# Optimization experiments

Hardware: AMD Instinct MI355X
Metric: run time of the kernel (lower is better)

The kernel has to match this reference:

```python
import jax, jax.numpy as jnp
import numpy as np

V = 50001   # vocab_size = len(word2id)+1
E = 256     # embedding_dim
H = 512     # hidden_dim (bi-LSTM output)
HD = 256    # hidden per direction = hidden_dim // 2
K = 9       # tagset_size
B = 64
T = 256


def setup_inputs() -> dict:
    key = jax.random.key(0)
    ks = jax.random.split(key, 16)
    n = lambda k, shape, s: (jax.random.normal(k, shape, jnp.float32) * s)
    inp = {
        "x": jax.random.randint(ks[0], (B, T), 0, V - 1),
        "embed": n(ks[1], (V, E), 0.1),
        # torch LSTM weights: gate order [i, f, g, o], each [4*HD, in]
        "w_ih_f": n(ks[2], (4 * HD, E), 0.05),
        "w_hh_f": n(ks[3], (4 * HD, HD), 0.05),
        "b_ih_f": n(ks[4], (4 * HD,), 0.05),
        "b_hh_f": n(ks[5], (4 * HD,), 0.05),
        "w_ih_b": n(ks[6], (4 * HD, E), 0.05),
        "w_hh_b": n(ks[7], (4 * HD, HD), 0.05),
        "b_ih_b": n(ks[8], (4 * HD,), 0.05),
        "b_hh_b": n(ks[9], (4 * HD,), 0.05),
        "w_out": n(ks[10], (K, H), 0.05),
        "b_out": n(ks[11], (K,), 0.05),
        "crf_start": n(ks[12], (K,), 0.1),
        "crf_end": n(ks[13], (K,), 0.1),
        "crf_trans": n(ks[14], (K, K), 0.1),
    }
    return inp


def _lstm_dir(xs, w_ih, w_hh, b_ih, b_hh, reverse):
    # xs: [T, B, E] -> hs: [T, B, HD]
    bsz = xs.shape[1]
    hd = w_hh.shape[1]
    b = b_ih + b_hh

    def step(carry, xt):
        h, c = carry
        g = xt @ w_ih.T + h @ w_hh.T + b
        i, f, gg, o = jnp.split(g, 4, axis=-1)
        c = jax.nn.sigmoid(f) * c + jax.nn.sigmoid(i) * jnp.tanh(gg)
        h = jax.nn.sigmoid(o) * jnp.tanh(c)
        return (h, c), h

    init = (jnp.zeros((bsz, hd), xs.dtype), jnp.zeros((bsz, hd), xs.dtype))
    _, hs = jax.lax.scan(step, init, xs, reverse=reverse)
    return hs


def _viterbi(emissions, start, trans, end):
    # emissions: [T, B, K] -> (best_score [B], path [B, T])
    score0 = start[None, :] + emissions[0]  # [B, K]

    def fwd(score, em_t):
        # score[b, i] + trans[i, j] + em_t[b, j]
        cand = score[:, :, None] + trans[None, :, :] + em_t[:, None, :]
        return jnp.max(cand, axis=1), jnp.argmax(cand, axis=1)  # [B,K], [B,K]

    final, history = jax.lax.scan(fwd, score0, emissions[1:])
    final = final + end[None, :]
    best_score = jnp.max(final, axis=-1)        # [B]
    last_tag = jnp.argmax(final, axis=-1)       # [B]

    def back(tag, hist_t):
        prev = jnp.take_along_axis(hist_t, tag[:, None], axis=1)[:, 0]
        return prev, prev

    _, tags_rev = jax.lax.scan(back, last_tag, history, reverse=True)
    path = jnp.concatenate([tags_rev, last_tag[None, :]], axis=0)  # [T, B]
    return best_score, path.T.astype(jnp.int32)


def reference(x, embed, w_ih_f, w_hh_f, b_ih_f, b_hh_f,
              w_ih_b, w_hh_b, b_ih_b, b_hh_b,
              w_out, b_out, crf_start, crf_end, crf_trans):
    xt = x.T                           # [T, B] time-major
    emb = embed[xt]                    # [T, B, E]
    h_f = _lstm_dir(emb, w_ih_f, w_hh_f, b_ih_f, b_hh_f, reverse=False)
    h_b = _lstm_dir(emb, w_ih_b, w_hh_b, b_ih_b, b_hh_b, reverse=True)
    h = jnp.concatenate([h_f, h_b], axis=-1)          # [T, B, H]
    # dropout is identity at inference (decode)
    emissions = jnp.einsum("tbh,kh->tbk", h, w_out) + b_out  # [T, B, K]
    best_score, path = _viterbi(emissions, crf_start, crf_trans, crf_end)
    return path, best_score
```

## Files before the change

kernel.cpp:

```cpp
#include <hip/hip_runtime.h>
#include <hip/hip_bf16.h>
#include <math.h>

#define VOCAB 50001
#define EDIM 256
#define HDIM 256
#define GDIM 1024
#define KTAG 9
#define NB 64
#define NT 256

static constexpr size_t XP_OFF   = 0;
static constexpr size_t HX_OFF   = XP_OFF + (size_t)16384*2048;
static constexpr size_t BIAS_OFF = HX_OFF + 131072;
static constexpr size_t HS_OFF   = BIAS_OFF + 2048;
static constexpr size_t EM_OFF   = HS_OFF + (size_t)16384*512;

#define FMA4(acc, W, H) acc += (W).x*(H).x + (W).y*(H).y + (W).z*(H).z + (W).w*(H).w

__global__ __launch_bounds__(256) void k_prep(const float* __restrict__ bif,
                                              const float* __restrict__ bhf,
                                              const float* __restrict__ bib,
                                              const float* __restrict__ bhb,
                                              float* __restrict__ ws) {
    int t = blockIdx.x * 256 + threadIdx.x;
    float* bias = ws + BIAS_OFF;
    if (t < 2048) {
        int d = t >> 10, g = t & 1023;
        bias[t] = d ? (bib[g] + bhb[g]) : (bif[g] + bhf[g]);
    }
    unsigned long long* hx = (unsigned long long*)(ws + HX_OFF);
    for (int i = t; i < 65536; i += 4096) hx[i] = 0ull;
}

#define BKC 32
__global__ __launch_bounds__(256) void k_xproj(const int* __restrict__ x,
                                               const float* __restrict__ embed,
                                               const float* __restrict__ wih_f,
                                               const float* __restrict__ wih_b,
                                               float* __restrict__ ws) {
    float* xp = ws + XP_OFF;
    const float* bias = ws + BIAS_OFF;
    __shared__ float As[BKC][68];
    __shared__ float Bs[BKC][68];
    __shared__ int ids[64];
    const int bm = blockIdx.x;
    const int bn = blockIdx.y;
    const int tid = threadIdx.x;
    const int tx = tid & 15, ty = tid >> 4;

    if (tid < 64) {
        int r = bm * 64 + tid;
        int t = r >> 6, b = r & 63;
        ids[tid] = x[b * 256 + t];
    }
    __syncthreads();

    float acc[4][4];
#pragma unroll
    for (int i = 0; i < 4; ++i)
#pragma unroll
        for (int j = 0; j < 4; ++j) acc[i][j] = 0.f;

    const int lm = tid >> 2;
    const int lks = (tid & 3) * 8;

    for (int k0 = 0; k0 < 256; k0 += BKC) {
        {
            const float* src = embed + (size_t)ids[lm] * 256 + k0 + lks;
            float4 a0 = *reinterpret_cast<const float4*>(src);
            float4 a1 = *reinterpret_cast<const float4*>(src + 4);
            As[lks + 0][lm] = a0.x; As[lks + 1][lm] = a0.y;
            As[lks + 2][lm] = a0.z; As[lks + 3][lm] = a0.w;
            As[lks + 4][lm] = a1.x; As[lks + 5][lm] = a1.y;
            As[lks + 6][lm] = a1.z; As[lks + 7][lm] = a1.w;
        }
        {
            int gn = bn * 64 + lm;
            const float* wsrc = (gn < 1024) ? (wih_f + (size_t)gn * 256)
                                            : (wih_b + (size_t)(gn - 1024) * 256);
            const float* src = wsrc + k0 + lks;
            float4 b0 = *reinterpret_cast<const float4*>(src);
            float4 b1 = *reinterpret_cast<const float4*>(src + 4);
            Bs[lks + 0][lm] = b0.x; Bs[lks + 1][lm] = b0.y;
            Bs[lks + 2][lm] = b0.z; Bs[lks + 3][lm] = b0.w;
            Bs[lks + 4][lm] = b1.x; Bs[lks + 5][lm] = b1.y;
            Bs[lks + 6][lm] = b1.z; Bs[lks + 7][lm] = b1.w;
        }
        __syncthreads();
#pragma unroll
        for (int k = 0; k < BKC; ++k) {
            float4 a = *reinterpret_cast<const float4*>(&As[k][ty * 4]);
            float4 bq = *reinterpret_cast<const float4*>(&Bs[k][tx * 4]);
            acc[0][0] += a.x * bq.x; acc[0][1] += a.x * bq.y; acc[0][2] += a.x * bq.z; acc[0][3] += a.x * bq.w;
            acc[1][0] += a.y * bq.x; acc[1][1] += a.y * bq.y; acc[1][2] += a.y * bq.z; acc[1][3] += a.y * bq.w;
            acc[2][0] += a.z * bq.x; acc[2][1] += a.z * bq.y; acc[2][2] += a.z * bq.z; acc[2][3] += a.z * bq.w;
            acc[3][0] += a.w * bq.x; acc[3][1] += a.w * bq.y; acc[3][2] += a.w * bq.z; acc[3][3] += a.w * bq.w;
        }
        __syncthreads();
    }

    const int gm = bm * 64 + ty * 4;
    const int gn = bn * 64 + tx * 4;
#pragma unroll
    for (int i = 0; i < 4; ++i) {
        float4 o;
        o.x = acc[i][0] + bias[gn + 0];
        o.y = acc[i][1] + bias[gn + 1];
        o.z = acc[i][2] + bias[gn + 2];
        o.w = acc[i][3] + bias[gn + 3];
        *reinterpret_cast<float4*>(xp + (size_t)(gm + i) * 2048 + gn) = o;
    }
}

#define WV 23
#define WL 9
#define REC_LDS_FLOATS (WL * 1024 * 4 + 256 + 512 + 512)

__global__ __launch_bounds__(1024)
__attribute__((amdgpu_waves_per_eu(4, 4)))
void k_rec3(const float* __restrict__ whh_f,
            const float* __restrict__ whh_b,
            float* __restrict__ ws) {
    extern __shared__ float sm[];
    float4* wlds4 = reinterpret_cast<float4*>(sm);
    float* hbuf = sm + WL * 1024 * 4;
    float* gact = hbuf + 256;
    float* psum = gact + 512;

    const float* xp = ws + XP_OFF;
    unsigned long long* hx = (unsigned long long*)(ws + HX_OFF);
    float* hs = ws + HS_OFF;

    const int blk = blockIdx.x;
    const int jhalf = blk >> 7;
    const int dir = (blk >> 6) & 1;
    const int batch = blk & 63;
    const int partner = blk ^ 128;
    const int t = threadIdx.x;
    const int kh = t >> 9;
    const int rr = t & 511;
    const int gt = rr >> 7;
    const int jj = rr & 127;
    const int row_global = gt * 256 + jhalf * 128 + jj;
    const int col = dir * 1024 + row_global;
    const float* wrow = (dir ? whh_b : whh_f) + (size_t)row_global * 256 + kh * 128;

    float4 w4[WV];
#pragma unroll
    for (int i = 0; i < WV; ++i) w4[i] = reinterpret_cast<const float4*>(wrow)[i];
#pragma unroll
    for (int c = 0; c < WL; ++c)
        wlds4[c * 1024 + t] = reinterpret_cast<const float4*>(wrow)[WV + c];

    if (t < 256) hbuf[t] = 0.f;
    float creg = 0.f;
    __syncthreads();

    const long xstep = dir ? -131072 : 131072;
    const long hstep = dir ? -32768 : 32768;
    const float* xptr = xp + (size_t)(dir ? 255 : 0) * 131072 + (size_t)batch * 2048 + col;
    float* hsptr = hs + (size_t)(dir ? 255 : 0) * 32768 + (size_t)batch * 512
                   + dir * 256 + jhalf * 128 + t;
    float xpv = (t < 512) ? *xptr : 0.f;

    for (int s = 0; s < 256; ++s) {
        const float* hk = hbuf + kh * 128;

        float a0 = 0.f, a1 = 0.f, a2 = 0.f, a3 = 0.f;
#pragma unroll
        for (int q = 0; q < WV; q += 4) {
            float4 h4;
            h4 = *reinterpret_cast<const float4*>(hk + (q + 0) * 4);
            FMA4(a0, w4[q + 0], h4);
            if (q + 1 < WV) { h4 = *reinterpret_cast<const float4*>(hk + (q + 1) * 4); FMA4(a1, w4[q + 1], h4); }
            if (q + 2 < WV) { h4 = *reinterpret_cast<const float4*>(hk + (q + 2) * 4); FMA4(a2, w4[q + 2], h4); }
            if (q + 3 < WV) { h4 = *reinterpret_cast<const float4*>(hk + (q + 3) * 4); FMA4(a3, w4[q + 3], h4); }
        }
#pragma unroll
        for (int c = 0; c < WL; ++c) {
            float4 h4 = *reinterpret_cast<const float4*>(hk + (WV + c) * 4);
            float4 wl = wlds4[c * 1024 + t];
            if ((c & 3) == 0) FMA4(a0, wl, h4);
            else if ((c & 3) == 1) FMA4(a1, wl, h4);
            else if ((c & 3) == 2) FMA4(a2, wl, h4);
            else FMA4(a3, wl, h4);
        }
        const float a = (a0 + a1) + (a2 + a3);

        if (kh) psum[rr] = a;
        __syncthreads();

        if (t < 512) {
            const float acc = xpv + a + psum[t];
            const float act = (gt == 2) ? tanhf(acc) : 1.f / (1.f + expf(-acc));
            gact[t] = act;
        }
        __syncthreads();

        if (t < 128) {
            const float si = gact[t], sf = gact[128 + t], tg = gact[256 + t], so = gact[384 + t];
            creg = sf * creg + si * tg;
            const float hval = so * tanhf(creg);
            const unsigned long long pk =
                ((unsigned long long)(unsigned)(s + 1) << 32) | (unsigned)__float_as_uint(hval);
            __hip_atomic_store(&hx[((size_t)(s & 1) * 256 + blk) * 128 + t], pk,
                               __ATOMIC_RELAXED, __HIP_MEMORY_SCOPE_AGENT);
            hbuf[jhalf * 128 + t] = hval;
            *hsptr = hval;
            hsptr += hstep;
        }

        if (t < 512 && s < 255) { xptr += xstep; xpv = *xptr; }

        if (t < 128) {
            unsigned long long u;
            do {
                u = __hip_atomic_load(&hx[((size_t)(s & 1) * 256 + partner) * 128 + t],
                                      __ATOMIC_RELAXED, __HIP_MEMORY_SCOPE_AGENT);
            } while ((unsigned)(u >> 32) != (unsigned)(s + 1));
            hbuf[(1 - jhalf) * 128 + t] = __uint_as_float((unsigned)u);
        }
        __syncthreads();
    }
}

__global__ __launch_bounds__(256) void k_emis(const float* __restrict__ wout,
                                              const float* __restrict__ bout,
                                              float* __restrict__ ws) {
    const float* hs = ws + HS_OFF;
    float* em = ws + EM_OFF;
    __shared__ float wl[9][512];
    __shared__ float bl[9];
    const int tid = threadIdx.x;
    for (int i = tid; i < 9 * 512; i += 256) wl[i / 512][i % 512] = wout[i];
    if (tid < 9) bl[tid] = bout[tid];
    __syncthreads();

    const int r = blockIdx.x * 256 + tid;
    const float4* hrow = reinterpret_cast<const float4*>(hs + (size_t)r * 512);
    float acc[9];
#pragma unroll
    for (int j = 0; j < 9; ++j) acc[j] = bl[j];
    for (int k4 = 0; k4 < 128; ++k4) {
        float4 h = hrow[k4];
#pragma unroll
        for (int j = 0; j < 9; ++j) {
            float4 w = *reinterpret_cast<const float4*>(&wl[j][k4 * 4]);
            acc[j] += h.x * w.x + h.y * w.y + h.z * w.z + h.w * w.w;
        }
    }
#pragma unroll
    for (int j = 0; j < 9; ++j) em[(size_t)r * 9 + j] = acc[j];
}

__global__ __launch_bounds__(64) void k_vit(const float* __restrict__ start,
                                            const float* __restrict__ endv,
                                            const float* __restrict__ trans,
                                            const float* __restrict__ ws_c,
                                            float* __restrict__ out) {
    const float* em = ws_c + EM_OFF;
    const int b = blockIdx.x;
    const int lane = threadIdx.x;
    __shared__ float tr[81];
    __shared__ float sc[9];
    __shared__ float ns[9];
    __shared__ int hist[256][9];

    for (int i = lane; i < 81; i += 64) tr[i] = trans[i];
    if (lane < 9) sc[lane] = start[lane] + em[(size_t)b * 9 + lane];
    __syncthreads();

    for (int t = 1; t < 256; ++t) {
        if (lane < 9) {
            float e = em[((size_t)t * 64 + b) * 9 + lane];
            float best = -1e30f; int bi = 0;
#pragma unroll
            for (int i = 0; i < 9; ++i) {
                float v = sc[i] + tr[i * 9 + lane];
                if (v > best) { best = v; bi = i; }
            }
            ns[lane] = best + e;
            hist[t][lane] = bi;
        }
        __syncthreads();
        if (lane < 9) sc[lane] = ns[lane];
        __syncthreads();
    }

    if (lane == 0) {
        float best = -1e30f; int bi = 0;
        for (int j = 0; j < 9; ++j) {
            float v = sc[j] + endv[j];
            if (v > best) { best = v; bi = j; }
        }
        out[16384 + b] = best;
        int cur = bi;
        out[(size_t)b * 256 + 255] = (float)cur;
        for (int t = 255; t >= 1; --t) {
            cur = hist[t][cur];
            out[(size_t)b * 256 + t - 1] = (float)cur;
        }
    }
}

extern "C" void kernel_launch(void* const* d_in, const int* in_sizes, int n_in,
                              void* d_out, int out_size, void* d_ws, size_t ws_size,
                              hipStream_t stream) {
    (void)in_sizes; (void)n_in; (void)out_size; (void)ws_size;
    const int*   x       = (const int*)d_in[0];
    const float* embed   = (const float*)d_in[1];
    const float* w_ih_f  = (const float*)d_in[2];
    const float* w_hh_f  = (const float*)d_in[3];
    const float* b_ih_f  = (const float*)d_in[4];
    const float* b_hh_f  = (const float*)d_in[5];
    const float* w_ih_b  = (const float*)d_in[6];
    const float* w_hh_b  = (const float*)d_in[7];
    const float* b_ih_b  = (const float*)d_in[8];
    const float* b_hh_b  = (const float*)d_in[9];
    const float* w_out   = (const float*)d_in[10];
    const float* b_out   = (const float*)d_in[11];
    const float* crf_start = (const float*)d_in[12];
    const float* crf_end   = (const float*)d_in[13];
    const float* crf_trans = (const float*)d_in[14];
    float* ws  = (float*)d_ws;
    float* out = (float*)d_out;

    const size_t rec_lds_bytes = (size_t)REC_LDS_FLOATS * 4;
    hipFuncSetAttribute(reinterpret_cast<const void*>(k_rec3),
                        hipFuncAttributeMaxDynamicSharedMemorySize,
                        (int)rec_lds_bytes);

    hipLaunchKernelGGL(k_prep, dim3(16), dim3(256), 0, stream,
                       b_ih_f, b_hh_f, b_ih_b, b_hh_b, ws);
    hipLaunchKernelGGL(k_xproj, dim3(256, 32), dim3(256), 0, stream,
                       x, embed, w_ih_f, w_ih_b, ws);
    hipLaunchKernelGGL(k_rec3, dim3(256), dim3(1024), rec_lds_bytes, stream,
                       w_hh_f, w_hh_b, ws);
    hipLaunchKernelGGL(k_emis, dim3(64), dim3(256), 0, stream, w_out, b_out, ws);
    hipLaunchKernelGGL(k_vit, dim3(64), dim3(64), 0, stream,
                       crf_start, crf_end, crf_trans, ws, out);
}
```

Before: 998.2 us.

## Process two batch elements per recurrent block to reuse register-held weights

The recurrent LSTM kernel now handles two batch rows per block, so each weight fragment held in registers and LDS serves two matvecs per timestep. The grid drops from 256 to 128 blocks, and the h-exchange buffers, gate buffers and cell states are duplicated. This amortises weight reads and the per-step barrier and partner-exchange cost over more work. In exchange each step has roughly twice the FMA and LDS-read work per block, and more register pressure at a fixed 4 waves/EU.

```diff
diff --git a/kernel.cpp b/kernel.cpp
--- a/kernel.cpp
+++ b/kernel.cpp
@@ -115,7 +115,7 @@
 
 #define WV 23
 #define WL 9
-#define REC_LDS_FLOATS (WL * 1024 * 4 + 256 + 512 + 512)
+#define REC_LDS_FLOATS (WL * 1024 * 4 + 2 * (256 + 512 + 512))
 
 __global__ __launch_bounds__(1024)
 __attribute__((amdgpu_waves_per_eu(4, 4)))
@@ -124,19 +124,23 @@
             float* __restrict__ ws) {
     extern __shared__ float sm[];
     float4* wlds4 = reinterpret_cast<float4*>(sm);
-    float* hbuf = sm + WL * 1024 * 4;
-    float* gact = hbuf + 256;
-    float* psum = gact + 512;
+    float* hbufA = sm + WL * 1024 * 4;
+    float* hbufB = hbufA + 256;
+    float* gactA = hbufB + 256;
+    float* gactB = gactA + 512;
+    float* psumA = gactB + 512;
+    float* psumB = psumA + 512;
 
     const float* xp = ws + XP_OFF;
     unsigned long long* hx = (unsigned long long*)(ws + HX_OFF);
     float* hs = ws + HS_OFF;
 
     const int blk = blockIdx.x;
-    const int jhalf = blk >> 7;
-    const int dir = (blk >> 6) & 1;
-    const int batch = blk & 63;
-    const int partner = blk ^ 128;
+    const int jhalf = blk >> 6;
+    const int dir = (blk >> 5) & 1;
+    const int bp = blk & 31;
+    const int bA = bp * 2, bB = bp * 2 + 1;
+    const int partner = blk ^ 64;
     const int t = threadIdx.x;
     const int kh = t >> 9;
     const int rr = t & 511;
@@ -153,73 +157,106 @@
     for (int c = 0; c < WL; ++c)
         wlds4[c * 1024 + t] = reinterpret_cast<const float4*>(wrow)[WV + c];
 
-    if (t < 256) hbuf[t] = 0.f;
-    float creg = 0.f;
+    if (t < 256) { hbufA[t] = 0.f; hbufB[t] = 0.f; }
+    float cregA = 0.f, cregB = 0.f;
     __syncthreads();
 
     const long xstep = dir ? -131072 : 131072;
     const long hstep = dir ? -32768 : 32768;
-    const float* xptr = xp + (size_t)(dir ? 255 : 0) * 131072 + (size_t)batch * 2048 + col;
-    float* hsptr = hs + (size_t)(dir ? 255 : 0) * 32768 + (size_t)batch * 512
-                   + dir * 256 + jhalf * 128 + t;
-    float xpv = (t < 512) ? *xptr : 0.f;
+    const float* xptrA = xp + (size_t)(dir ? 255 : 0) * 131072 + (size_t)bA * 2048 + col;
+    const float* xptrB = xp + (size_t)(dir ? 255 : 0) * 131072 + (size_t)bB * 2048 + col;
+    float* hsA = hs + (size_t)(dir ? 255 : 0) * 32768 + (size_t)bA * 512
+                 + dir * 256 + jhalf * 128 + t;
+    float* hsB = hs + (size_t)(dir ? 255 : 0) * 32768 + (size_t)bB * 512
+                 + dir * 256 + jhalf * 128 + t;
+    float xpvA = (t < 512) ? *xptrA : 0.f;
+    float xpvB = (t < 512) ? *xptrB : 0.f;
 
     for (int s = 0; s < 256; ++s) {
-        const float* hk = hbuf + kh * 128;
-
-        float a0 = 0.f, a1 = 0.f, a2 = 0.f, a3 = 0.f;
+        const float* hkA = hbufA + kh * 128;
+        const float* hkB = hbufB + kh * 128;
+
+        float a0A = 0.f, a1A = 0.f, a2A = 0.f, a3A = 0.f;
+        float a0B = 0.f, a1B = 0.f, a2B = 0.f, a3B = 0.f;
+        float4 h4;
 #pragma unroll
         for (int q = 0; q < WV; q += 4) {
-            float4 h4;
-            h4 = *reinterpret_cast<const float4*>(hk + (q + 0) * 4);
-            FMA4(a0, w4[q + 0], h4);
-            if (q + 1 < WV) { h4 = *reinterpret_cast<const float4*>(hk + (q + 1) * 4); FMA4(a1, w4[q + 1], h4); }
-            if (q + 2 < WV) { h4 = *reinterpret_cast<const float4*>(hk + (q + 2) * 4); FMA4(a2, w4[q + 2], h4); }
-            if (q + 3 < WV) { h4 = *reinterpret_cast<const float4*>(hk + (q + 3) * 4); FMA4(a3, w4[q + 3], h4); }
+            h4 = *reinterpret_cast<const float4*>(hkA + (q + 0) * 4); FMA4(a0A, w4[q + 0], h4);
+            h4 = *reinterpret_cast<const float4*>(hkB + (q + 0) * 4); FMA4(a0B, w4[q + 0], h4);
+            if (q + 1 < WV) {
+                h4 = *reinterpret_cast<const float4*>(hkA + (q + 1) * 4); FMA4(a1A, w4[q + 1], h4);
+                h4 = *reinterpret_cast<const float4*>(hkB + (q + 1) * 4); FMA4(a1B, w4[q + 1], h4);
+            }
+            if (q + 2 < WV) {
+                h4 = *reinterpret_cast<const float4*>(hkA + (q + 2) * 4); FMA4(a2A, w4[q + 2], h4);
+                h4 = *reinterpret_cast<const float4*>(hkB + (q + 2) * 4); FMA4(a2B, w4[q + 2], h4);
+            }
+            if (q + 3 < WV) {
+                h4 = *reinterpret_cast<const float4*>(hkA + (q + 3) * 4); FMA4(a3A, w4[q + 3], h4);
+                h4 = *reinterpret_cast<const float4*>(hkB + (q + 3) * 4); FMA4(a3B, w4[q + 3], h4);
+            }
         }
 #pragma unroll
         for (int c = 0; c < WL; ++c) {
-            float4 h4 = *reinterpret_cast<const float4*>(hk + (WV + c) * 4);
             float4 wl = wlds4[c * 1024 + t];
-            if ((c & 3) == 0) FMA4(a0, wl, h4);
-            else if ((c & 3) == 1) FMA4(a1, wl, h4);
-            else if ((c & 3) == 2) FMA4(a2, wl, h4);
-            else FMA4(a3, wl, h4);
-        }
-        const float a = (a0 + a1) + (a2 + a3);
-
-        if (kh) psum[rr] = a;
+            float4 hA = *reinterpret_cast<const float4*>(hkA + (WV + c) * 4);
+            float4 hB = *reinterpret_cast<const float4*>(hkB + (WV + c) * 4);
+            if ((c & 3) == 0)      { FMA4(a0A, wl, hA); FMA4(a0B, wl, hB); }
+            else if ((c & 3) == 1) { FMA4(a1A, wl, hA); FMA4(a1B, wl, hB); }
+            else if ((c & 3) == 2) { FMA4(a2A, wl, hA); FMA4(a2B, wl, hB); }
+            else                   { FMA4(a3A, wl, hA); FMA4(a3B, wl, hB); }
+        }
+        const float aA = (a0A + a1A) + (a2A + a3A);
+        const float aB = (a0B + a1B) + (a2B + a3B);
+
+        if (kh) { psumA[rr] = aA; psumB[rr] = aB; }
         __syncthreads();
 
         if (t < 512) {
-            const float acc = xpv + a + psum[t];
-            const float act = (gt == 2) ? tanhf(acc) : 1.f / (1.f + expf(-acc));
-            gact[t] = act;
+            const float accA = xpvA + aA + psumA[t];
+            const float accB = xpvB + aB + psumB[t];
+            gactA[t] = (gt == 2) ? tanhf(accA) : 1.f / (1.f + expf(-accA));
+            gactB[t] = (gt == 2) ? tanhf(accB) : 1.f / (1.f + expf(-accB));
         }
         __syncthreads();
 
         if (t < 128) {
-            const float si = gact[t], sf = gact[128 + t], tg = gact[256 + t], so = gact[384 + t];
-            creg = sf * creg + si * tg;
-            const float hval = so * tanhf(creg);
-            const unsigned long long pk =
-                ((unsigned long long)(unsigned)(s + 1) << 32) | (unsigned)__float_as_uint(hval);
-            __hip_atomic_store(&hx[((size_t)(s & 1) * 256 + blk) * 128 + t], pk,
+            const float siA = gactA[t], sfA = gactA[128 + t], tgA = gactA[256 + t], soA = gactA[384 + t];
+            cregA = sfA * cregA + siA * tgA;
+            const float hvA = soA * tanhf(cregA);
+            const float siB = gactB[t], sfB = gactB[128 + t], tgB = gactB[256 + t], soB = gactB[384 + t];
+            cregB = sfB * cregB + siB * tgB;
+            const float hvB = soB * tanhf(cregB);
+            const unsigned tagv = (unsigned)(s + 1);
+            __hip_atomic_store(&hx[((size_t)(s & 1) * 256 + blk * 2 + 0) * 128 + t],
+                               ((unsigned long long)tagv << 32) | (unsigned)__float_as_uint(hvA),
                                __ATOMIC_RELAXED, __HIP_MEMORY_SCOPE_AGENT);
-            hbuf[jhalf * 128 + t] = hval;
-            *hsptr = hval;
-            hsptr += hstep;
-        }
-
-        if (t < 512 && s < 255) { xptr += xstep; xpv = *xptr; }
+            __hip_atomic_store(&hx[((size_t)(s & 1) * 256 + blk * 2 + 1) * 128 + t],
+                               ((unsigned long long)tagv << 32) | (unsigned)__float_as_uint(hvB),
+                               __ATOMIC_RELAXED, __HIP_MEMORY_SCOPE_AGENT);
+            hbufA[jhalf * 128 + t] = hvA;
+            hbufB[jhalf * 128 + t] = hvB;
+            *hsA = hvA; hsA += hstep;
+            *hsB = hvB; hsB += hstep;
+        }
+
+        if (t < 512 && s < 255) {
+            xptrA += xstep; xpvA = *xptrA;
+            xptrB += xstep; xpvB = *xptrB;
+        }
 
         if (t < 128) {
             unsigned long long u;
             do {
-                u = __hip_atomic_load(&hx[((size_t)(s & 1) * 256 + partner) * 128 + t],
+                u = __hip_atomic_load(&hx[((size_t)(s & 1) * 256 + partner * 2 + 0) * 128 + t],
                                       __ATOMIC_RELAXED, __HIP_MEMORY_SCOPE_AGENT);
             } while ((unsigned)(u >> 32) != (unsigned)(s + 1));
-            hbuf[(1 - jhalf) * 128 + t] = __uint_as_float((unsigned)u);
+            hbufA[(1 - jhalf) * 128 + t] = __uint_as_float((unsigned)u);
+            do {
+                u = __hip_atomic_load(&hx[((size_t)(s & 1) * 256 + partner * 2 + 1) * 128 + t],
+                                      __ATOMIC_RELAXED, __HIP_MEMORY_SCOPE_AGENT);
+            } while ((unsigned)(u >> 32) != (unsigned)(s + 1));
+            hbufB[(1 - jhalf) * 128 + t] = __uint_as_float((unsigned)u);
         }
         __syncthreads();
     }
@@ -335,7 +372,7 @@
                        b_ih_f, b_hh_f, b_ih_b, b_hh_b, ws);
     hipLaunchKernelGGL(k_xproj, dim3(256, 32), dim3(256), 0, stream,
                        x, embed, w_ih_f, w_ih_b, ws);
-    hipLaunchKernelGGL(k_rec3, dim3(256), dim3(1024), rec_lds_bytes, stream,
+    hipLaunchKernelGGL(k_rec3, dim3(128), dim3(1024), rec_lds_bytes, stream,
                        w_hh_f, w_hh_b, ws);
     hipLaunchKernelGGL(k_emis, dim3(64), dim3(256), 0, stream, w_out, b_out, ws);
     hipLaunchKernelGGL(k_vit, dim3(64), dim3(64), 0, stream,
```

Measured after the change: 1.846 ms. 1.85x slower.
